# Optimization experiments

Measured on AMD Instinct MI355X. Metric: run time of the kernel, lower is better.

Reference implementation:

```python
import jax, jax.numpy as jnp
import numpy as np

DIM_EMB = 1024
DIM_K = 128
DIM_V = 128
BATCH = 4
SEQ = 4096

def setup_inputs() -> dict:
    key = jax.random.key(0)
    kx, kq, kk, kv = jax.random.split(key, 4)
    x = jax.random.normal(kx, (BATCH, SEQ, DIM_EMB), dtype=jnp.float32)
    Wq = jax.random.normal(kq, (DIM_EMB, DIM_K), dtype=jnp.float32) * (1.0 / np.sqrt(DIM_EMB))
    Wk = jax.random.normal(kk, (DIM_EMB, DIM_K), dtype=jnp.float32) * (1.0 / np.sqrt(DIM_EMB))
    Wv = jax.random.normal(kv, (DIM_EMB, DIM_V), dtype=jnp.float32) * (1.0 / np.sqrt(DIM_EMB))
    return {"x": x, "Wq": Wq, "Wk": Wk, "Wv": Wv}

def reference(x, Wq, Wk, Wv):
    # x: [b, s, e]; projections (torch Linear without bias -> x @ W)
    seq_len = x.shape[1]
    q = x @ Wq  # [b, s, dk]
    k = x @ Wk  # [b, s, dk]
    v = x @ Wv  # [b, s, dv]
    # NOTE: original scales by 1/sqrt(dim_emb), not 1/sqrt(dim_k)
    scale = 1.0 / np.sqrt(x.shape[-1])
    qk = jnp.einsum('bqd,bkd->bqk', q, k) * scale  # [b, s, s]
    causal = jnp.tril(jnp.ones((seq_len, seq_len), dtype=bool))
    masked_qk = jnp.where(causal, qk, -jnp.inf)
    att = jax.nn.softmax(masked_qk, axis=-1)  # dropout p=0.0 -> identity
    return att @ v  # [b, s, dv]
```

## Files before the change

### kernel.cpp

```cpp
#include <hip/hip_runtime.h>

typedef __attribute__((ext_vector_type(8))) short s8v;
typedef __attribute__((ext_vector_type(4))) short s4v;
typedef __attribute__((ext_vector_type(4))) float f4v;

#define S_ 4096
#define E_ 1024
#define D_ 128

__device__ __forceinline__ unsigned short f2bf(float f) {
  unsigned int u = __float_as_uint(f);
  return (unsigned short)((u + 0x7FFFu + ((u >> 16) & 1u)) >> 16);
}

__global__ __launch_bounds__(256) void zero_kernel(float* __restrict__ p) {
  const int i = blockIdx.x * 256 + threadIdx.x;
  float4 z = {0.f, 0.f, 0.f, 0.f};
  reinterpret_cast<float4*>(p)[i] = z;
}

__global__ __launch_bounds__(256) void wcvt_kernel(
    const float* __restrict__ Wq, const float* __restrict__ Wk,
    const float* __restrict__ Wv, unsigned short* __restrict__ Wt) {
  __shared__ unsigned short T[64][72];
  const int p = blockIdx.y;
  const float* W = (p == 0) ? Wq : (p == 1) ? Wk : Wv;
  const int k0 = (blockIdx.x >> 1) * 64;
  const int n0 = (blockIdx.x & 1) * 64;
  const int t = threadIdx.x, rr = t >> 4, c4 = (t & 15) * 4;
#pragma unroll
  for (int i = 0; i < 4; ++i) {
    int kr = i * 16 + rr;
    float4 w = *reinterpret_cast<const float4*>(W + (size_t)(k0 + kr) * D_ + n0 + c4);
    T[c4 + 0][kr] = f2bf(w.x); T[c4 + 1][kr] = f2bf(w.y);
    T[c4 + 2][kr] = f2bf(w.z); T[c4 + 3][kr] = f2bf(w.w);
  }
  __syncthreads();
#pragma unroll
  for (int i = 0; i < 4; ++i) {
    int n = i * 16 + rr;
    s4v v;
    v[0] = (short)T[n][c4]; v[1] = (short)T[n][c4 + 1];
    v[2] = (short)T[n][c4 + 2]; v[3] = (short)T[n][c4 + 3];
    *reinterpret_cast<s4v*>(Wt + (size_t)(p * D_ + n0 + n) * E_ + k0 + c4) = v;
  }
}

__global__ __launch_bounds__(256) void proj_kernel(
    const float* __restrict__ x, const unsigned short* __restrict__ Wt,
    unsigned short* __restrict__ Qb, unsigned short* __restrict__ Kb,
    unsigned short* __restrict__ VT) {
  __shared__ __align__(16) unsigned short As[64 * 72];
  __shared__ __align__(16) unsigned short Bs[128 * 72];
  const int bid = blockIdx.x;
  const int cls = bid & 7, j = bid >> 3;
  const int m0 = (cls * 32 + j / 3) * 64, ng = j % 3;
  const int t = threadIdx.x;
  const int wv = t >> 6, lane = t & 63, quad = lane >> 4, l16 = lane & 15;
  const int wr = wv >> 1, wc = wv & 1;

  f4v acc[2][4];
  const f4v fz = {0.f, 0.f, 0.f, 0.f};
#pragma unroll
  for (int i = 0; i < 2; ++i)
#pragma unroll
    for (int k = 0; k < 4; ++k) acc[i][k] = fz;

  const int arow = t >> 2, aq = t & 3;
  const int brow = t >> 1, bh = t & 1;
  const float* xg = x + (size_t)(m0 + arow) * E_ + aq * 16;
  const unsigned short* wg = Wt + (size_t)(ng * 128 + brow) * E_ + bh * 32;

  float4 xa[4];
  s8v wb[4];
#pragma unroll
  for (int i = 0; i < 4; ++i) xa[i] = *reinterpret_cast<const float4*>(xg + i * 4);
#pragma unroll
  for (int i = 0; i < 4; ++i) wb[i] = *reinterpret_cast<const s8v*>(wg + i * 8);

  for (int kk = 0; kk < E_; kk += 64) {
    __syncthreads();
#pragma unroll
    for (int i = 0; i < 2; ++i) {
      s8v av;
      av[0] = (short)f2bf(xa[2 * i].x);     av[1] = (short)f2bf(xa[2 * i].y);
      av[2] = (short)f2bf(xa[2 * i].z);     av[3] = (short)f2bf(xa[2 * i].w);
      av[4] = (short)f2bf(xa[2 * i + 1].x); av[5] = (short)f2bf(xa[2 * i + 1].y);
      av[6] = (short)f2bf(xa[2 * i + 1].z); av[7] = (short)f2bf(xa[2 * i + 1].w);
      *reinterpret_cast<s8v*>(As + arow * 72 + aq * 16 + i * 8) = av;
    }
#pragma unroll
    for (int i = 0; i < 4; ++i)
      *reinterpret_cast<s8v*>(Bs + brow * 72 + bh * 32 + i * 8) = wb[i];
    __syncthreads();
    if (kk + 64 < E_) {
#pragma unroll
      for (int i = 0; i < 4; ++i)
        xa[i] = *reinterpret_cast<const float4*>(xg + kk + 64 + i * 4);
#pragma unroll
      for (int i = 0; i < 4; ++i)
        wb[i] = *reinterpret_cast<const s8v*>(wg + kk + 64 + i * 8);
    }
#pragma unroll
    for (int ks = 0; ks < 2; ++ks) {
      s8v af[2], bf[4];
#pragma unroll
      for (int rt = 0; rt < 2; ++rt)
        af[rt] = *reinterpret_cast<const s8v*>(
            As + (wr * 32 + rt * 16 + l16) * 72 + ks * 32 + quad * 8);
#pragma unroll
      for (int ct = 0; ct < 4; ++ct)
        bf[ct] = *reinterpret_cast<const s8v*>(
            Bs + (wc * 64 + ct * 16 + l16) * 72 + ks * 32 + quad * 8);
#pragma unroll
      for (int rt = 0; rt < 2; ++rt)
#pragma unroll
        for (int ct = 0; ct < 4; ++ct)
          acc[rt][ct] = __builtin_amdgcn_mfma_f32_16x16x32_bf16(
              af[rt], bf[ct], acc[rt][ct], 0, 0, 0);
    }
  }

  if (ng < 2) {
    unsigned short* dst = ng ? Kb : Qb;
#pragma unroll
    for (int rt = 0; rt < 2; ++rt)
#pragma unroll
      for (int ct = 0; ct < 4; ++ct)
#pragma unroll
        for (int r = 0; r < 4; ++r)
          dst[(size_t)(m0 + wr * 32 + rt * 16 + quad * 4 + r) * D_ +
              wc * 64 + ct * 16 + l16] = f2bf(acc[rt][ct][r]);
  } else {
    const int b = m0 >> 12;
    const int s0 = (m0 & (S_ - 1)) + wr * 32;
#pragma unroll
    for (int rt = 0; rt < 2; ++rt)
#pragma unroll
      for (int ct = 0; ct < 4; ++ct) {
        s4v v;
        v[0] = (short)f2bf(acc[rt][ct][0]); v[1] = (short)f2bf(acc[rt][ct][1]);
        v[2] = (short)f2bf(acc[rt][ct][2]); v[3] = (short)f2bf(acc[rt][ct][3]);
        *reinterpret_cast<s4v*>(
            VT + ((size_t)b * D_ + wc * 64 + ct * 16 + l16) * S_ + s0 +
            rt * 16 + quad * 4) = v;
      }
  }
}

__global__ __launch_bounds__(256, 4) void flash_kernel(
    const unsigned short* __restrict__ Qb, const unsigned short* __restrict__ Kb,
    const unsigned short* __restrict__ VT, float* __restrict__ Oacc,
    float* __restrict__ Lacc) {
  __shared__ __align__(16) unsigned short KS[64 * 128];
  __shared__ __align__(16) unsigned short VS[128 * 72];
  const int id = blockIdx.x;
  const int xcd = id & 7;
  const int b = xcd >> 1;
  const int sub = 287 - ((id >> 3) * 2 + (xcd & 1));
  int g = 0;
#pragma unroll
  for (int gg = 0; gg < 7; ++gg)
    if (sub >= 4 * (gg + 1) * (gg + 2)) g = gg + 1;
  const int off = sub - 4 * g * (g + 1);
  const int qt = 8 * g + off / (g + 1);
  const int s = off % (g + 1);
  const int q0 = qt * 64;
  const int klo = s * 512;
  const int khi = min((s + 1) * 512, (qt + 1) * 64);

  const int t = threadIdx.x;
  const int wv = t >> 6, lane = t & 63, quad = lane >> 4, l16 = lane & 15;
  const int qrow0 = q0 + wv * 16;
  const float SCL2 = 0.03125f * 1.44269504088896340736f;

  const unsigned short* Kbb = Kb + (size_t)b * S_ * D_;
  const unsigned short* Vbb = VT + (size_t)b * D_ * S_;

  s8v Qf[4];
#pragma unroll
  for (int ks = 0; ks < 4; ++ks)
    Qf[ks] = *reinterpret_cast<const s8v*>(
        Qb + ((size_t)b * S_ + qrow0 + l16) * D_ + ks * 32 + quad * 8);

  f4v O[8];
  const f4v fz = {0.f, 0.f, 0.f, 0.f};
#pragma unroll
  for (int nt = 0; nt < 8; ++nt) O[nt] = fz;
  float lt = 0.f;

  const int krow = t >> 4, kgb = t & 15;
  const int vrow = t >> 1, vgb = (t & 1) * 4;

  s8v kr[4], vr[4];
#pragma unroll
  for (int i = 0; i < 4; ++i) {
    kr[i] = *reinterpret_cast<const s8v*>(
        Kbb + (size_t)(klo + krow + 16 * i) * D_ + kgb * 8);
    vr[i] = *reinterpret_cast<const s8v*>(
        Vbb + (size_t)vrow * S_ + klo + (vgb + i) * 8);
  }

  for (int k0 = klo; k0 < khi; k0 += 64) {
    __syncthreads();
#pragma unroll
    for (int i = 0; i < 4; ++i) {
      const int r = krow + 16 * i;
      const int sig = (krow & 3) | ((((krow >> 3) + 2 * i) & 3) << 2);
      *reinterpret_cast<s8v*>(KS + r * 128 + ((kgb ^ sig) * 8)) = kr[i];
      *reinterpret_cast<s8v*>(VS + vrow * 72 + (vgb + i) * 8) = vr[i];
    }
    __syncthreads();
    if (k0 + 64 < khi) {
#pragma unroll
      for (int i = 0; i < 4; ++i) {
        kr[i] = *reinterpret_cast<const s8v*>(
            Kbb + (size_t)(k0 + 64 + krow + 16 * i) * D_ + kgb * 8);
        vr[i] = *reinterpret_cast<const s8v*>(
            Vbb + (size_t)vrow * S_ + k0 + 64 + (vgb + i) * 8);
      }
    }

    if (k0 <= qrow0 + 15) {
      f4v St[2][2];
#pragma unroll
      for (int c = 0; c < 2; ++c)
#pragma unroll
        for (int s2 = 0; s2 < 2; ++s2) St[c][s2] = fz;
#pragma unroll
      for (int ks = 0; ks < 4; ++ks)
#pragma unroll
        for (int c = 0; c < 2; ++c)
#pragma unroll
          for (int s2 = 0; s2 < 2; ++s2) {
            const int row = c * 32 + ((l16 >> 2) << 3) + s2 * 4 + (l16 & 3);
            s8v kf = *reinterpret_cast<const s8v*>(
                KS + row * 128 + (((ks * 4 + quad) ^ l16) * 8));
            St[c][s2] = __builtin_amdgcn_mfma_f32_16x16x32_bf16(
                kf, Qf[ks], St[c][s2], 0, 0, 0);
          }
      const bool full = (k0 + 63 <= qrow0);
      s8v pf[2];
#pragma unroll
      for (int c = 0; c < 2; ++c) {
        float ladd = 0.f;
#pragma unroll
        for (int s2 = 0; s2 < 2; ++s2)
#pragma unroll
          for (int r = 0; r < 4; ++r) {
            float e = exp2f(St[c][s2][r] * SCL2);
            if (!full) {
              int key = k0 + c * 32 + quad * 8 + s2 * 4 + r;
              if (key > qrow0 + l16) e = 0.f;
            }
            ladd += e;
            pf[c][s2 * 4 + r] = (short)f2bf(e);
          }
        lt += ladd;
      }
#pragma unroll
      for (int c = 0; c < 2; ++c)
#pragma unroll
        for (int nt = 0; nt < 8; ++nt) {
          s8v vf = *reinterpret_cast<const s8v*>(
              VS + (nt * 16 + l16) * 72 + (c * 4 + quad) * 8);
          O[nt] = __builtin_amdgcn_mfma_f32_16x16x32_bf16(
              pf[c], vf, O[nt], 0, 0, 0);
        }
    }
  }

  lt += __shfl_xor(lt, 16);
  lt += __shfl_xor(lt, 32);
  float* Ob = Oacc + (size_t)b * S_ * D_;
#pragma unroll
  for (int nt = 0; nt < 8; ++nt)
#pragma unroll
    for (int r = 0; r < 4; ++r)
      atomicAdd(&Ob[(size_t)(qrow0 + quad * 4 + r) * D_ + nt * 16 + l16],
                O[nt][r]);
  if (lane < 16) atomicAdd(&Lacc[(size_t)b * S_ + qrow0 + l16], lt);
}

__global__ __launch_bounds__(256) void norm_kernel(
    const float* __restrict__ Oacc, const float* __restrict__ Lacc,
    float* __restrict__ out) {
  const int idx = blockIdx.x * 256 + threadIdx.x;
  const int base = idx * 4;
  const int row = base >> 7;
  float4 o = reinterpret_cast<const float4*>(Oacc)[idx];
  float L = Lacc[row];
  float4 r;
  r.x = o.x / L; r.y = o.y / L; r.z = o.z / L; r.w = o.w / L;
  reinterpret_cast<float4*>(out)[idx] = r;
}

extern "C" void kernel_launch(void* const* d_in, const int* in_sizes, int n_in,
                              void* d_out, int out_size, void* d_ws, size_t ws_size,
                              hipStream_t stream) {
  const float* x = (const float*)d_in[0];
  const float* Wq = (const float*)d_in[1];
  const float* Wk = (const float*)d_in[2];
  const float* Wv = (const float*)d_in[3];
  float* out = (float*)d_out;

  char* ws = (char*)d_ws;
  unsigned short* Qb = (unsigned short*)ws;
  unsigned short* Kb = (unsigned short*)(ws + (((size_t)4) << 20));
  unsigned short* VT = (unsigned short*)(ws + (((size_t)8) << 20));
  unsigned short* Wt = (unsigned short*)(ws + (((size_t)12) << 20));
  float* Oacc = (float*)(ws + (((size_t)13) << 20));
  float* Lacc = (float*)(ws + (((size_t)21) << 20));

  zero_kernel<<<2064, 256, 0, stream>>>(Oacc);
  wcvt_kernel<<<dim3(32, 3), 256, 0, stream>>>(Wq, Wk, Wv, Wt);
  proj_kernel<<<768, 256, 0, stream>>>(x, Wt, Qb, Kb, VT);
  flash_kernel<<<1152, 256, 0, stream>>>(Qb, Kb, VT, Oacc, Lacc);
  norm_kernel<<<2048, 256, 0, stream>>>(Oacc, Lacc, out);
}
```

Before: 197.9 us.

## Pre-convert x to bf16 and stage projection tiles via direct global-to-LDS loads

```diff
diff --git a/kernel.cpp b/kernel.cpp
--- a/kernel.cpp
+++ b/kernel.cpp
@@ -11,12 +11,31 @@
 __device__ __forceinline__ unsigned short f2bf(float f) {
   unsigned int u = __float_as_uint(f);
   return (unsigned short)((u + 0x7FFFu + ((u >> 16) & 1u)) >> 16);
+}
+
+__device__ __forceinline__ void gload16(const void* g, void* l) {
+  __builtin_amdgcn_global_load_lds(
+      (const __attribute__((address_space(1))) unsigned int*)g,
+      (__attribute__((address_space(3))) unsigned int*)l, 16, 0, 0);
 }
 
 __global__ __launch_bounds__(256) void zero_kernel(float* __restrict__ p) {
   const int i = blockIdx.x * 256 + threadIdx.x;
   float4 z = {0.f, 0.f, 0.f, 0.f};
   reinterpret_cast<float4*>(p)[i] = z;
+}
+
+__global__ __launch_bounds__(256) void xcvt_kernel(
+    const float* __restrict__ x, unsigned short* __restrict__ Xb) {
+  const size_t i = ((size_t)blockIdx.x * 256 + threadIdx.x) * 8;
+  float4 a = *reinterpret_cast<const float4*>(x + i);
+  float4 b = *reinterpret_cast<const float4*>(x + i + 4);
+  s8v v;
+  v[0] = (short)f2bf(a.x); v[1] = (short)f2bf(a.y);
+  v[2] = (short)f2bf(a.z); v[3] = (short)f2bf(a.w);
+  v[4] = (short)f2bf(b.x); v[5] = (short)f2bf(b.y);
+  v[6] = (short)f2bf(b.z); v[7] = (short)f2bf(b.w);
+  *reinterpret_cast<s8v*>(Xb + i) = v;
 }
 
 __global__ __launch_bounds__(256) void wcvt_kernel(
@@ -47,95 +66,79 @@
 }
 
 __global__ __launch_bounds__(256) void proj_kernel(
-    const float* __restrict__ x, const unsigned short* __restrict__ Wt,
+    const unsigned short* __restrict__ Xb, const unsigned short* __restrict__ Wt,
     unsigned short* __restrict__ Qb, unsigned short* __restrict__ Kb,
     unsigned short* __restrict__ VT) {
-  __shared__ __align__(16) unsigned short As[64 * 72];
-  __shared__ __align__(16) unsigned short Bs[128 * 72];
+  __shared__ __align__(16) unsigned short As[128 * 64];
+  __shared__ __align__(16) unsigned short Bs[128 * 64];
   const int bid = blockIdx.x;
   const int cls = bid & 7, j = bid >> 3;
-  const int m0 = (cls * 32 + j / 3) * 64, ng = j % 3;
+  const int m0 = (cls * 16 + j / 3) * 128, ng = j % 3;
   const int t = threadIdx.x;
   const int wv = t >> 6, lane = t & 63, quad = lane >> 4, l16 = lane & 15;
   const int wr = wv >> 1, wc = wv & 1;
 
-  f4v acc[2][4];
+  f4v acc[4][4];
   const f4v fz = {0.f, 0.f, 0.f, 0.f};
 #pragma unroll
-  for (int i = 0; i < 2; ++i)
+  for (int i = 0; i < 4; ++i)
 #pragma unroll
     for (int k = 0; k < 4; ++k) acc[i][k] = fz;
 
-  const int arow = t >> 2, aq = t & 3;
-  const int brow = t >> 1, bh = t & 1;
-  const float* xg = x + (size_t)(m0 + arow) * E_ + aq * 16;
-  const unsigned short* wg = Wt + (size_t)(ng * 128 + brow) * E_ + bh * 32;
-
-  float4 xa[4];
-  s8v wb[4];
-#pragma unroll
-  for (int i = 0; i < 4; ++i) xa[i] = *reinterpret_cast<const float4*>(xg + i * 4);
-#pragma unroll
-  for (int i = 0; i < 4; ++i) wb[i] = *reinterpret_cast<const s8v*>(wg + i * 8);
+  const int rbase = wv * 32 + (lane >> 3);
+  const int scb = ((lane & 7) ^ (lane >> 3)) * 16;
+  const char* aSrc = (const char*)(Xb + (size_t)(m0 + rbase) * E_) + scb;
+  const char* bSrc = (const char*)(Wt + (size_t)(ng * 128 + rbase) * E_) + scb;
+  char* aDst = (char*)As + wv * 4096;
+  char* bDst = (char*)Bs + wv * 4096;
+
+  const int xm = (l16 & 7) * 16;
+  const char* Ab = (const char*)As + (wr * 64 + l16) * 128;
+  const char* Bb = (const char*)Bs + (wc * 64 + l16) * 128;
 
   for (int kk = 0; kk < E_; kk += 64) {
+#pragma unroll
+    for (int i = 0; i < 4; ++i)
+      gload16(aSrc + (size_t)i * (8 * E_ * 2) + kk * 2, aDst + i * 1024);
+#pragma unroll
+    for (int i = 0; i < 4; ++i)
+      gload16(bSrc + (size_t)i * (8 * E_ * 2) + kk * 2, bDst + i * 1024);
     __syncthreads();
 #pragma unroll
-    for (int i = 0; i < 2; ++i) {
-      s8v av;
-      av[0] = (short)f2bf(xa[2 * i].x);     av[1] = (short)f2bf(xa[2 * i].y);
-      av[2] = (short)f2bf(xa[2 * i].z);     av[3] = (short)f2bf(xa[2 * i].w);
-      av[4] = (short)f2bf(xa[2 * i + 1].x); av[5] = (short)f2bf(xa[2 * i + 1].y);
-      av[6] = (short)f2bf(xa[2 * i + 1].z); av[7] = (short)f2bf(xa[2 * i + 1].w);
-      *reinterpret_cast<s8v*>(As + arow * 72 + aq * 16 + i * 8) = av;
-    }
-#pragma unroll
-    for (int i = 0; i < 4; ++i)
-      *reinterpret_cast<s8v*>(Bs + brow * 72 + bh * 32 + i * 8) = wb[i];
-    __syncthreads();
-    if (kk + 64 < E_) {
-#pragma unroll
-      for (int i = 0; i < 4; ++i)
-        xa[i] = *reinterpret_cast<const float4*>(xg + kk + 64 + i * 4);
-#pragma unroll
-      for (int i = 0; i < 4; ++i)
-        wb[i] = *reinterpret_cast<const s8v*>(wg + kk + 64 + i * 8);
-    }
-#pragma unroll
     for (int ks = 0; ks < 2; ++ks) {
-      s8v af[2], bf[4];
-#pragma unroll
-      for (int rt = 0; rt < 2; ++rt)
-        af[rt] = *reinterpret_cast<const s8v*>(
-            As + (wr * 32 + rt * 16 + l16) * 72 + ks * 32 + quad * 8);
+      const int co = (ks * 64 + quad * 16) ^ xm;
+      s8v af[4], bf[4];
+#pragma unroll
+      for (int rt = 0; rt < 4; ++rt)
+        af[rt] = *reinterpret_cast<const s8v*>(Ab + rt * 16 * 128 + co);
 #pragma unroll
       for (int ct = 0; ct < 4; ++ct)
-        bf[ct] = *reinterpret_cast<const s8v*>(
-            Bs + (wc * 64 + ct * 16 + l16) * 72 + ks * 32 + quad * 8);
-#pragma unroll
-      for (int rt = 0; rt < 2; ++rt)
+        bf[ct] = *reinterpret_cast<const s8v*>(Bb + ct * 16 * 128 + co);
+#pragma unroll
+      for (int rt = 0; rt < 4; ++rt)
 #pragma unroll
         for (int ct = 0; ct < 4; ++ct)
           acc[rt][ct] = __builtin_amdgcn_mfma_f32_16x16x32_bf16(
               af[rt], bf[ct], acc[rt][ct], 0, 0, 0);
     }
+    __syncthreads();
   }
 
   if (ng < 2) {
     unsigned short* dst = ng ? Kb : Qb;
 #pragma unroll
-    for (int rt = 0; rt < 2; ++rt)
+    for (int rt = 0; rt < 4; ++rt)
 #pragma unroll
       for (int ct = 0; ct < 4; ++ct)
 #pragma unroll
         for (int r = 0; r < 4; ++r)
-          dst[(size_t)(m0 + wr * 32 + rt * 16 + quad * 4 + r) * D_ +
+          dst[(size_t)(m0 + wr * 64 + rt * 16 + quad * 4 + r) * D_ +
               wc * 64 + ct * 16 + l16] = f2bf(acc[rt][ct][r]);
   } else {
     const int b = m0 >> 12;
-    const int s0 = (m0 & (S_ - 1)) + wr * 32;
-#pragma unroll
-    for (int rt = 0; rt < 2; ++rt)
+    const int s0 = (m0 & (S_ - 1)) + wr * 64;
+#pragma unroll
+    for (int rt = 0; rt < 4; ++rt)
 #pragma unroll
       for (int ct = 0; ct < 4; ++ct) {
         s4v v;
@@ -309,12 +312,14 @@
   unsigned short* Kb = (unsigned short*)(ws + (((size_t)4) << 20));
   unsigned short* VT = (unsigned short*)(ws + (((size_t)8) << 20));
   unsigned short* Wt = (unsigned short*)(ws + (((size_t)12) << 20));
+  unsigned short* Xb = (unsigned short*)(ws + (((size_t)13) << 20));
   float* Oacc = (float*)(ws + (((size_t)13) << 20));
   float* Lacc = (float*)(ws + (((size_t)21) << 20));
 
+  wcvt_kernel<<<dim3(32, 3), 256, 0, stream>>>(Wq, Wk, Wv, Wt);
+  xcvt_kernel<<<8192, 256, 0, stream>>>(x, Xb);
+  proj_kernel<<<384, 256, 0, stream>>>(Xb, Wt, Qb, Kb, VT);
   zero_kernel<<<2064, 256, 0, stream>>>(Oacc);
-  wcvt_kernel<<<dim3(32, 3), 256, 0, stream>>>(Wq, Wk, Wv, Wt);
-  proj_kernel<<<768, 256, 0, stream>>>(x, Wt, Qb, Kb, VT);
   flash_kernel<<<1152, 256, 0, stream>>>(Qb, Kb, VT, Oacc, Lacc);
   norm_kernel<<<2048, 256, 0, stream>>>(Oacc, Lacc, out);
 }
```

Result: no change. 200.2 us (+1.1%).
